# Kernel optimization log

Hardware: AMD Instinct MI355X
Metric: run time of the kernel (lower is better)

Reference implementation:

```python
import jax, jax.numpy as jnp
import numpy as np

S, H, K, B, T = 128, 512, 16, 2048, 67  # state, hidden, bm, batch(paths), len(ts)


def _lin(key, i, o):
    kw, kb = jax.random.split(key)
    w = jax.random.normal(kw, (i, o), jnp.float32) / np.sqrt(i).astype(np.float32)
    b = jax.random.normal(kb, (o,), jnp.float32) * 0.01
    return w, b


def setup_inputs() -> dict:
    key = jax.random.key(0)
    ks = jax.random.split(key, 10)
    enc_w1, enc_b1 = _lin(ks[0], 3, H)
    enc_w2, enc_b2 = _lin(ks[1], H, S)
    f_w1, f_b1 = _lin(ks[2], S + 1, H)
    f_w2, f_b2 = _lin(ks[3], H, H)
    f_w3, f_b3 = _lin(ks[4], H, S)
    g_w1, g_b1 = _lin(ks[5], S + 1, H)
    g_w2, g_b2 = _lin(ks[6], H, S * K)
    ts = jnp.linspace(0.0, 1.0, T, dtype=jnp.float32)
    x = jax.random.normal(ks[7], (B, 3), jnp.float32)
    # standard-normal Brownian increments; scaled by sqrt(dt) inside reference
    dW = jax.random.normal(ks[8], (T - 4, B, K), jnp.float32)
    return dict(ts=ts, x=x,
                enc_w1=enc_w1, enc_b1=enc_b1, enc_w2=enc_w2, enc_b2=enc_b2,
                f_w1=f_w1, f_b1=f_b1, f_w2=f_w2, f_b2=f_b2, f_w3=f_w3, f_b3=f_b3,
                g_w1=g_w1, g_b1=g_b1, g_w2=g_w2, g_b2=g_b2, dW=dW)


def reference(ts, x, enc_w1, enc_b1, enc_w2, enc_b2,
              f_w1, f_b1, f_w2, f_b2, f_w3, f_b3,
              g_w1, g_b1, g_w2, g_b2, dW):
    Bn = x.shape[0]
    Sn = enc_w2.shape[1]
    Kn = dW.shape[-1]

    # encoder: y0 = MLP(x)  -> [B, S]
    y0 = jax.nn.relu(x @ enc_w1 + enc_b1) @ enc_w2 + enc_b2

    ts_sol = ts[3:]                      # solve grid, length T-3
    dts = ts_sol[1:] - ts_sol[:-1]       # [T-4]
    dWs = dW * jnp.sqrt(dts)[:, None, None]  # Brownian increments ~ N(0, dt)

    def with_time(t, y):  # concat scalar time onto state -> [B, S+1]
        tcol = jnp.broadcast_to(jnp.reshape(t, (1, 1)), (Bn, 1)).astype(y.dtype)
        return jnp.concatenate([tcol, y], axis=-1)

    def drift(t, y):  # f(t,y): [B,S]
        h = jax.nn.relu(with_time(t, y) @ f_w1 + f_b1)
        h = jax.nn.relu(h @ f_w2 + f_b2)
        return h @ f_w3 + f_b3

    def g_prod(t, y, dw):  # g(t,y) @ dW : [B,S]
        h = jax.nn.relu(with_time(t, y) @ g_w1 + g_b1)
        g = (h @ g_w2 + g_b2).reshape(Bn, Sn, Kn)
        return jnp.einsum('bsk,bk->bs', g, dw)

    def step(y, inp):  # euler_heun (Stratonovich): Euler drift + Heun diffusion
        t, dt, dw = inp
        gp = g_prod(t, y, dw)
        gp_prime = g_prod(t, y + gp, dw)
        y1 = y + drift(t, y) * dt + 0.5 * (gp + gp_prime)
        return y1, y1

    _, ys = jax.lax.scan(step, y0, (ts_sol[:-1], dts, dWs))
    sol = jnp.concatenate([y0[None], ys], axis=0)  # [T-3, B, S]
    return sol.reshape(-1)
```

## Files before the change

kernel.cpp:

```cpp
#include <hip/hip_runtime.h>
#include <hip/hip_bf16.h>
#include <math.h>

#define B_  2048
#define S_  128
#define H_  512
#define K_  16
#define NSTEP 63

typedef __bf16 bf16x8 __attribute__((ext_vector_type(8)));
typedef float  f32x4  __attribute__((ext_vector_type(4)));
typedef unsigned short u16x8 __attribute__((ext_vector_type(8)));

static __device__ __forceinline__ void f2b2(float v, unsigned short& hi, unsigned short& lo)
{
    __hip_bfloat16 h = __float2bfloat16(v);
    float r = v - __bfloat162float(h);
    __hip_bfloat16 l = __float2bfloat16(r);
    hi = __builtin_bit_cast(unsigned short, h);
    lo = __builtin_bit_cast(unsigned short, l);
}

static __device__ __forceinline__ void gl16(const unsigned short* g, unsigned short* l)
{
    __builtin_amdgcn_global_load_lds(
        (const __attribute__((address_space(1))) unsigned int*)g,
        (__attribute__((address_space(3))) unsigned int*)l, 16, 0, 0);
}

template<int BM,int BN,int BK,int WM,int WN>
__device__ __forceinline__ void gemm_core(
    unsigned short* lds,
    const unsigned short* __restrict__ Ahi, const unsigned short* __restrict__ Alo, int lda,
    const unsigned short* __restrict__ Whi, const unsigned short* __restrict__ Wlo, int K,
    int rowBase, int colBase, f32x4 (&acc)[WM/16][WN/16])
{
    constexpr int MI = WM/16, NJ = WN/16, NWC = BN/WN;
    constexpr int NT = (BM/WM)*(BN/WN)*64;
    constexpr int ACH = BM*BK/8, BCH = BN*BK/8;
    unsigned short* Ah = lds;
    unsigned short* Al = lds + (size_t)ACH*8;
    unsigned short* Bh = lds + (size_t)2*ACH*8;
    unsigned short* Bl = lds + (size_t)2*ACH*8 + (size_t)BCH*8;

    const int tid = threadIdx.x, lane = tid & 63;
    const int wid = tid >> 6;
    const int wr = wid / NWC, wc = wid % NWC;
    const int r16 = lane & 15, kg = lane >> 4;
    const int ubase = tid & ~63;

    for (int k0 = 0; k0 < K; k0 += BK) {
#pragma unroll
        for (int c0 = 0; c0 < ACH; c0 += NT) {
            int c = c0 + tid;
            int row = c % BM, g = c / BM;
            size_t off = (size_t)(rowBase + row) * lda + k0 + g*8;
            gl16(Ahi + off, Ah + (size_t)(c0 + ubase)*8);
            gl16(Alo + off, Al + (size_t)(c0 + ubase)*8);
        }
#pragma unroll
        for (int c0 = 0; c0 < BCH; c0 += NT) {
            int c = c0 + tid;
            int row = c % BN, g = c / BN;
            size_t off = (size_t)(colBase + row) * K + k0 + g*8;
            gl16(Whi + off, Bh + (size_t)(c0 + ubase)*8);
            gl16(Wlo + off, Bl + (size_t)(c0 + ubase)*8);
        }
        __syncthreads();
#pragma unroll
        for (int kk = 0; kk < BK/32; ++kk) {
            bf16x8 ah[MI], al[MI], bh[NJ], bl[NJ];
#pragma unroll
            for (int i = 0; i < MI; ++i) {
                int idx = (kk*4 + kg)*BM + wr*WM + i*16 + r16;
                ah[i] = __builtin_bit_cast(bf16x8, *(const u16x8*)(Ah + (size_t)idx*8));
                al[i] = __builtin_bit_cast(bf16x8, *(const u16x8*)(Al + (size_t)idx*8));
            }
#pragma unroll
            for (int j = 0; j < NJ; ++j) {
                int idx = (kk*4 + kg)*BN + wc*WN + j*16 + r16;
                bh[j] = __builtin_bit_cast(bf16x8, *(const u16x8*)(Bh + (size_t)idx*8));
                bl[j] = __builtin_bit_cast(bf16x8, *(const u16x8*)(Bl + (size_t)idx*8));
            }
#pragma unroll
            for (int i = 0; i < MI; ++i)
#pragma unroll
                for (int j = 0; j < NJ; ++j) {
                    acc[i][j] = __builtin_amdgcn_mfma_f32_16x16x32_bf16(ah[i], bh[j], acc[i][j], 0, 0, 0);
                    acc[i][j] = __builtin_amdgcn_mfma_f32_16x16x32_bf16(ah[i], bl[j], acc[i][j], 0, 0, 0);
                    acc[i][j] = __builtin_amdgcn_mfma_f32_16x16x32_bf16(al[i], bh[j], acc[i][j], 0, 0, 0);
                }
        }
        __syncthreads();
    }
}


__global__ __launch_bounds__(256) void k1_phase(
    const unsigned short* __restrict__ ycH, const unsigned short* __restrict__ ycL,
    const unsigned short* __restrict__ w1tH, const unsigned short* __restrict__ w1tL,
    const float* __restrict__ g_w1, const float* __restrict__ f_w1,
    const float* __restrict__ g_b1, const float* __restrict__ f_b1,
    const float* __restrict__ ts, int step,
    unsigned short* __restrict__ HAh, unsigned short* __restrict__ HAl)
{
    constexpr int BM=64, BN=128, WM=32, WN=64, MI=2, NJ=4, NWC=BN/WN;
    __shared__ __align__(16) unsigned short lds[(BM+BN)*64*2];
    f32x4 acc[MI][NJ] = {};
    const int rowBase = blockIdx.x*BM, colBase = blockIdx.y*BN;
    gemm_core<BM,BN,64,WM,WN>(lds, ycH, ycL, S_, w1tH, w1tL, S_, rowBase, colBase, acc);

    const int tid=threadIdx.x, l=tid&63, wid=tid>>6;
    const int wr=wid/NWC, wc=wid%NWC, r16=l&15, rg=l>>4;
    const float t = ts[3+step];
#pragma unroll
    for (int j=0;j<NJ;++j){
        int colj = colBase + wc*WN + j*16 + r16;
        float be = (colj < 512) ? (g_b1[colj] + t*g_w1[colj])
                                : (f_b1[colj-512] + t*f_w1[colj-512]);
#pragma unroll
        for (int i=0;i<MI;++i)
#pragma unroll
            for (int reg=0;reg<4;++reg){
                int row = rowBase + wr*WM + i*16 + rg*4 + reg;
                float v = fmaxf(acc[i][j][reg] + be, 0.f);
                unsigned short h,lo; f2b2(v,h,lo);
                size_t o = (size_t)row*1024 + colj;
                HAh[o]=h; HAl[o]=lo;
            }
    }
}

__global__ __launch_bounds__(256) void k2_phase(
    const unsigned short* __restrict__ HAh, const unsigned short* __restrict__ HAl,
    const unsigned short* __restrict__ gw2H, const unsigned short* __restrict__ gw2L,
    const unsigned short* __restrict__ fw2H, const unsigned short* __restrict__ fw2L,
    const float* __restrict__ g_b2, const float* __restrict__ f_b2,
    const float* __restrict__ y,
    const float* __restrict__ dWs,
    const float* __restrict__ ts, int step,
    float* __restrict__ gp,
    unsigned short* __restrict__ ytH, unsigned short* __restrict__ ytL,
    unsigned short* __restrict__ HBh, unsigned short* __restrict__ HBl)
{
    constexpr int BM=64, BN=128, WM=32, WN=64, MI=2, NJ=4, NWC=BN/WN;
    __shared__ __align__(16) unsigned short lds[(BM+BN)*64*2];
    f32x4 acc[MI][NJ] = {};
    const int rowBase = blockIdx.x*BM;
    const int by = blockIdx.y;
    const int tid=threadIdx.x, l=tid&63, wid=tid>>6;
    const int wr=wid/NWC, wc=wid%NWC, r16=l&15, rg=l>>4;

    if (by < 16) {
        const int colBase = by*BN;
        gemm_core<BM,BN,64,WM,WN>(lds, HAh, HAl, 1024, gw2H, gw2L, H_, rowBase, colBase, acc);
        const float dt = ts[4+step]-ts[3+step], sq = sqrtf(dt);
#pragma unroll
        for (int i=0;i<MI;++i)
#pragma unroll
            for (int reg=0;reg<4;++reg){
                int row = rowBase + wr*WM + i*16 + rg*4 + reg;
                float dwv = dWs[row*K_ + r16] * sq;
#pragma unroll
                for (int j=0;j<NJ;++j){
                    int colj = colBase + wc*WN + j*16;
                    float m = (acc[i][j][reg] + g_b2[colj + r16]) * dwv;
                    m += __shfl_xor(m,1); m += __shfl_xor(m,2);
                    m += __shfl_xor(m,4); m += __shfl_xor(m,8);
                    if (r16 == 0){
                        int idx = row*S_ + (colj>>4);
                        gp[idx] = m;
                        unsigned short h,lo; f2b2(y[idx] + m, h, lo);
                        ytH[idx]=h; ytL[idx]=lo;
                    }
                }
            }
    } else {
        const int colBase = (by-16)*BN;
        gemm_core<BM,BN,64,WM,WN>(lds, HAh + 512, HAl + 512, 1024, fw2H, fw2L, H_, rowBase, colBase, acc);
#pragma unroll
        for (int j=0;j<NJ;++j){
            int colj = colBase + wc*WN + j*16 + r16;
            float be = f_b2[colj];
#pragma unroll
            for (int i=0;i<MI;++i)
#pragma unroll
                for (int reg=0;reg<4;++reg){
                    int row = rowBase + wr*WM + i*16 + rg*4 + reg;
                    float v = fmaxf(acc[i][j][reg] + be, 0.f);
                    unsigned short h,lo; f2b2(v,h,lo);
                    size_t o = (size_t)row*512 + colj;
                    HBh[o]=h; HBl[o]=lo;
                }
        }
    }
}

__global__ __launch_bounds__(256) void k3_phase(
    const unsigned short* __restrict__ ytH, const unsigned short* __restrict__ ytL,
    const unsigned short* __restrict__ w1tH, const unsigned short* __restrict__ w1tL,
    const float* __restrict__ g_b1, const float* __restrict__ g_w1,
    const unsigned short* __restrict__ HBh, const unsigned short* __restrict__ HBl,
    const unsigned short* __restrict__ fw3H, const unsigned short* __restrict__ fw3L,
    const float* __restrict__ f_b3,
    const float* __restrict__ ts, int step,
    unsigned short* __restrict__ HA2h, unsigned short* __restrict__ HA2l,
    float* __restrict__ drift)
{
    constexpr int BM=64, BN=64, WM=32, WN=32, MI=2, NJ=2, NWC=BN/WN;
    __shared__ __align__(16) unsigned short lds[(BM+BN)*64*2];
    f32x4 acc[MI][NJ] = {};
    const int rowBase = blockIdx.x*BM;
    const int by = blockIdx.y;
    const int tid=threadIdx.x, l=tid&63, wid=tid>>6;
    const int wr=wid/NWC, wc=wid%NWC, r16=l&15, rg=l>>4;

    if (by < 8) {
        const int colBase = by*BN;
        gemm_core<BM,BN,64,WM,WN>(lds, ytH, ytL, S_, w1tH, w1tL, S_, rowBase, colBase, acc);
        const float t = ts[3+step];
#pragma unroll
        for (int j=0;j<NJ;++j){
            int colj = colBase + wc*WN + j*16 + r16;
            float be = g_b1[colj] + t*g_w1[colj];
#pragma unroll
            for (int i=0;i<MI;++i)
#pragma unroll
                for (int reg=0;reg<4;++reg){
                    int row = rowBase + wr*WM + i*16 + rg*4 + reg;
                    float v = fmaxf(acc[i][j][reg] + be, 0.f);
                    unsigned short h,lo; f2b2(v,h,lo);
                    size_t o = (size_t)row*512 + colj;
                    HA2h[o]=h; HA2l[o]=lo;
                }
        }
    } else {
        const int colBase = (by-8)*BN;
        gemm_core<BM,BN,64,WM,WN>(lds, HBh, HBl, H_, fw3H, fw3L, H_, rowBase, colBase, acc);
#pragma unroll
        for (int j=0;j<NJ;++j){
            int colj = colBase + wc*WN + j*16 + r16;
            float be = f_b3[colj];
#pragma unroll
            for (int i=0;i<MI;++i)
#pragma unroll
                for (int reg=0;reg<4;++reg){
                    int row = rowBase + wr*WM + i*16 + rg*4 + reg;
                    drift[row*S_ + colj] = acc[i][j][reg] + be;
                }
        }
    }
}

__global__ __launch_bounds__(256) void k4_phase(
    const unsigned short* __restrict__ HA2h, const unsigned short* __restrict__ HA2l,
    const unsigned short* __restrict__ gw2H, const unsigned short* __restrict__ gw2L,
    const float* __restrict__ g_b2,
    const float* __restrict__ y,
    const float* __restrict__ gp,
    const float* __restrict__ drift,
    const float* __restrict__ dWs,
    const float* __restrict__ ts, int step,
    float* __restrict__ y1,
    unsigned short* __restrict__ ycH, unsigned short* __restrict__ ycL)
{
    constexpr int BM=64, BN=128, WM=32, WN=64, MI=2, NJ=4, NWC=BN/WN;
    __shared__ __align__(16) unsigned short lds[(BM+BN)*64*2];
    f32x4 acc[MI][NJ] = {};
    const int rowBase = blockIdx.x*BM;
    const int colBase = blockIdx.y*BN;
    gemm_core<BM,BN,64,WM,WN>(lds, HA2h, HA2l, H_, gw2H, gw2L, H_, rowBase, colBase, acc);

    const int tid=threadIdx.x, l=tid&63, wid=tid>>6;
    const int wr=wid/NWC, wc=wid%NWC, r16=l&15, rg=l>>4;
    const float dt = ts[4+step]-ts[3+step], sq = sqrtf(dt);
#pragma unroll
    for (int i=0;i<MI;++i)
#pragma unroll
        for (int reg=0;reg<4;++reg){
            int row = rowBase + wr*WM + i*16 + rg*4 + reg;
            float dwv = dWs[row*K_ + r16] * sq;
#pragma unroll
            for (int j=0;j<NJ;++j){
                int colj = colBase + wc*WN + j*16;
                float m = (acc[i][j][reg] + g_b2[colj + r16]) * dwv;
                m += __shfl_xor(m,1); m += __shfl_xor(m,2);
                m += __shfl_xor(m,4); m += __shfl_xor(m,8);
                if (r16 == 0){
                    int idx = row*S_ + (colj>>4);
                    float v1 = y[idx] + drift[idx]*dt + 0.5f*(gp[idx] + m);
                    y1[idx] = v1;
                    unsigned short h,lo; f2b2(v1,h,lo);
                    ycH[idx]=h; ycL[idx]=lo;
                }
            }
        }
}

__global__ __launch_bounds__(256) void tcast_k(
    const float* __restrict__ in, int rowOff, int Kd, int N,
    unsigned short* __restrict__ outH, unsigned short* __restrict__ outL)
{
    __shared__ float tl[32][33];
    const int kb = blockIdx.x*32, nb = blockIdx.y*32;
    const int tx = threadIdx.x, ty = threadIdx.y;
    for (int r = ty; r < 32; r += 8)
        tl[r][tx] = in[(size_t)(rowOff + kb + r)*N + nb + tx];
    __syncthreads();
    for (int r = ty; r < 32; r += 8){
        unsigned short h,lo; f2b2(tl[tx][r],h,lo);
        size_t o = (size_t)(nb + r)*Kd + kb + tx;
        outH[o]=h; outL[o]=lo;
    }
}

__global__ __launch_bounds__(128) void encoder_k(
    const float* __restrict__ x,
    const float* __restrict__ w1, const float* __restrict__ b1,
    const float* __restrict__ w2, const float* __restrict__ b2,
    float* __restrict__ y0,
    unsigned short* __restrict__ ycH, unsigned short* __restrict__ ycL)
{
    int b = blockIdx.x;
    __shared__ float h[H_];
    int tid = threadIdx.x;
    float x0 = x[b*3+0], x1 = x[b*3+1], x2 = x[b*3+2];
    for (int i = tid; i < H_; i += 128)
        h[i] = fmaxf(x0*w1[i] + x1*w1[H_+i] + x2*w1[2*H_+i] + b1[i], 0.f);
    __syncthreads();
    float acc = b2[tid];
    for (int k = 0; k < H_; ++k) acc += h[k]*w2[k*S_+tid];
    size_t o = (size_t)b*S_ + tid;
    y0[o] = acc;
    unsigned short hh,ll; f2b2(acc,hh,ll);
    ycH[o]=hh; ycL[o]=ll;
}

extern "C" void kernel_launch(void* const* d_in, const int* in_sizes, int n_in,
                              void* d_out, int out_size, void* d_ws, size_t ws_size,
                              hipStream_t stream)
{
    const float* ts     = (const float*)d_in[0];
    const float* x      = (const float*)d_in[1];
    const float* enc_w1 = (const float*)d_in[2];
    const float* enc_b1 = (const float*)d_in[3];
    const float* enc_w2 = (const float*)d_in[4];
    const float* enc_b2 = (const float*)d_in[5];
    const float* f_w1   = (const float*)d_in[6];
    const float* f_b1   = (const float*)d_in[7];
    const float* f_w2   = (const float*)d_in[8];
    const float* f_b2   = (const float*)d_in[9];
    const float* f_w3   = (const float*)d_in[10];
    const float* f_b3   = (const float*)d_in[11];
    const float* g_w1   = (const float*)d_in[12];
    const float* g_b1   = (const float*)d_in[13];
    const float* g_w2   = (const float*)d_in[14];
    const float* g_b2   = (const float*)d_in[15];
    const float* dW     = (const float*)d_in[16];

    float* out = (float*)d_out;
    unsigned short* w = (unsigned short*)d_ws;

    unsigned short* w1tH  = w;
    unsigned short* w1tL  = w1tH  + 1024*128;
    unsigned short* gw2H  = w1tL  + 1024*128;
    unsigned short* gw2L  = gw2H  + 2048*512;
    unsigned short* fw2H  = gw2L  + 2048*512;
    unsigned short* fw2L  = fw2H  + 512*512;
    unsigned short* fw3H  = fw2L  + 512*512;
    unsigned short* fw3L  = fw3H  + 128*512;
    unsigned short* HAh   = fw3L  + 128*512;
    unsigned short* HAl   = HAh   + 2048*1024;
    unsigned short* HBh   = HAl   + 2048*1024;
    unsigned short* HBl   = HBh   + 2048*512;
    unsigned short* ytH   = HBl   + 2048*512;
    unsigned short* ytL   = ytH   + 2048*128;
    unsigned short* ycH   = ytL   + 2048*128;
    unsigned short* ycL   = ycH   + 2048*128;
    float* gp    = (float*)(ycL + 2048*128);
    float* drift = gp + 2048*128;
    unsigned short* HA2h = HAh;
    unsigned short* HA2l = HAl;

    dim3 tb(32,8);
    tcast_k<<<dim3(4,16),  tb, 0, stream>>>(g_w1, 1, 128, 512,  w1tH,          w1tL);
    tcast_k<<<dim3(4,16),  tb, 0, stream>>>(f_w1, 1, 128, 512,  w1tH+512*128,  w1tL+512*128);
    tcast_k<<<dim3(16,16), tb, 0, stream>>>(f_w2, 0, 512, 512,  fw2H,          fw2L);
    tcast_k<<<dim3(16,4),  tb, 0, stream>>>(f_w3, 0, 512, 128,  fw3H,          fw3L);
    tcast_k<<<dim3(16,64), tb, 0, stream>>>(g_w2, 0, 512, 2048, gw2H,          gw2L);

    encoder_k<<<B_, 128, 0, stream>>>(x, enc_w1, enc_b1, enc_w2, enc_b2, out, ycH, ycL);

    for (int step = 0; step < NSTEP; ++step) {
        const float* y   = out + (size_t)step * B_ * S_;
        float*       y1  = out + (size_t)(step+1) * B_ * S_;
        const float* dWs = dW  + (size_t)step * B_ * K_;

        k1_phase<<<dim3(32,8),  256, 0, stream>>>(ycH, ycL, w1tH, w1tL, g_w1, f_w1,
                                                  g_b1, f_b1, ts, step, HAh, HAl);
        k2_phase<<<dim3(32,20), 256, 0, stream>>>(HAh, HAl, gw2H, gw2L, fw2H, fw2L,
                                                  g_b2, f_b2, y, dWs, ts, step,
                                                  gp, ytH, ytL, HBh, HBl);
        k3_phase<<<dim3(32,10), 256, 0, stream>>>(ytH, ytL, w1tH, w1tL, g_b1, g_w1,
                                                  HBh, HBl, fw3H, fw3L, f_b3, ts, step,
                                                  HA2h, HA2l, drift);
        k4_phase<<<dim3(32,16), 256, 0, stream>>>(HA2h, HA2l, gw2H, gw2L, g_b2,
                                                  y, gp, drift, dWs, ts, step,
                                                  y1, ycH, ycL);
    }
}
```

Before: 7.322 ms.

## Double-buffer LDS tiles in GEMM core, enlarge tiles, swizzle block order

Rewrites the shared split-bf16 GEMM core to double-buffer LDS tiles, issuing the next K-tile's global-to-LDS loads while MFMAs run on the current one, with one barrier per tile. The k2 and k4 GEMMs move to 128x128 tiles, k3 uses 64x128 tiles, and all launches become 1D grids remapped so consecutive blocks spread across column strips. The aim is to hide global-load latency and improve weight reuse in L2. In exchange it doubles LDS use and sets launch_bounds to one block per CU, and the larger tiles give k2 and k4 fewer blocks than before.

Measured after the change: 10.34 ms. 1.41x slower.

```diff
diff --git a/kernel.cpp b/kernel.cpp
--- a/kernel.cpp
+++ b/kernel.cpp
@@ -28,75 +28,110 @@
         (__attribute__((address_space(3))) unsigned int*)l, 16, 0, 0);
 }
 
-template<int BM,int BN,int BK,int WM,int WN>
-__device__ __forceinline__ void gemm_core(
+
+template<int BM>
+static __device__ __forceinline__ void stage_tile(
+    const unsigned short* __restrict__ Ahi, const unsigned short* __restrict__ Alo, int lda,
+    const unsigned short* __restrict__ Whi, const unsigned short* __restrict__ Wlo, int K,
+    int rowBase, int colBase, int k0, unsigned short* buf, int tid)
+{
+    constexpr int PLA = BM*64, PLB = 128*64;
+    unsigned short* Ah = buf;
+    unsigned short* Al = buf + PLA;
+    unsigned short* Bh = buf + 2*PLA;
+    unsigned short* Bl = buf + 2*PLA + PLB;
+    const int ub = tid & ~63;
+#pragma unroll
+    for (int c0 = 0; c0 < BM*8; c0 += 256) {
+        int c = c0 + tid;
+        int row = c % BM, g = c / BM;
+        size_t off = (size_t)(rowBase + row) * lda + k0 + g*8;
+        gl16(Ahi + off, Ah + (size_t)(c0 + ub)*8);
+        gl16(Alo + off, Al + (size_t)(c0 + ub)*8);
+    }
+#pragma unroll
+    for (int c0 = 0; c0 < 1024; c0 += 256) {
+        int c = c0 + tid;
+        int row = c & 127, g = c >> 7;
+        size_t off = (size_t)(colBase + row) * K + k0 + g*8;
+        gl16(Whi + off, Bh + (size_t)(c0 + ub)*8);
+        gl16(Wlo + off, Bl + (size_t)(c0 + ub)*8);
+    }
+}
+
+template<int BM>
+static __device__ __forceinline__ void read_frags(
+    const unsigned short* buf, int kk, int wr, int wc, int r16, int kg,
+    bf16x8 (&a_h)[BM/32], bf16x8 (&a_l)[BM/32], bf16x8 (&b_h)[4], bf16x8 (&b_l)[4])
+{
+    constexpr int MI = BM/32;
+    constexpr int PLA = BM*64, PLB = 128*64;
+    const unsigned short* Ah = buf;
+    const unsigned short* Al = buf + PLA;
+    const unsigned short* Bh = buf + 2*PLA;
+    const unsigned short* Bl = buf + 2*PLA + PLB;
+#pragma unroll
+    for (int i = 0; i < MI; ++i) {
+        int ch = (kk*4 + kg)*BM + wr*(BM/2) + i*16 + r16;
+        a_h[i] = __builtin_bit_cast(bf16x8, *(const u16x8*)(Ah + (size_t)ch*8));
+        a_l[i] = __builtin_bit_cast(bf16x8, *(const u16x8*)(Al + (size_t)ch*8));
+    }
+#pragma unroll
+    for (int j = 0; j < 4; ++j) {
+        int ch = (kk*4 + kg)*128 + wc*64 + j*16 + r16;
+        b_h[j] = __builtin_bit_cast(bf16x8, *(const u16x8*)(Bh + (size_t)ch*8));
+        b_l[j] = __builtin_bit_cast(bf16x8, *(const u16x8*)(Bl + (size_t)ch*8));
+    }
+}
+
+template<int MI>
+static __device__ __forceinline__ void do_mfma(
+    const bf16x8 (&a_h)[MI], const bf16x8 (&a_l)[MI],
+    const bf16x8 (&b_h)[4], const bf16x8 (&b_l)[4], f32x4 (&acc)[MI][4])
+{
+#pragma unroll
+    for (int i = 0; i < MI; ++i)
+#pragma unroll
+        for (int j = 0; j < 4; ++j) {
+            acc[i][j] = __builtin_amdgcn_mfma_f32_16x16x32_bf16(a_h[i], b_h[j], acc[i][j], 0, 0, 0);
+            acc[i][j] = __builtin_amdgcn_mfma_f32_16x16x32_bf16(a_h[i], b_l[j], acc[i][j], 0, 0, 0);
+            acc[i][j] = __builtin_amdgcn_mfma_f32_16x16x32_bf16(a_l[i], b_h[j], acc[i][j], 0, 0, 0);
+        }
+}
+
+template<int BM>
+static __device__ __forceinline__ void gemm_core(
     unsigned short* lds,
     const unsigned short* __restrict__ Ahi, const unsigned short* __restrict__ Alo, int lda,
     const unsigned short* __restrict__ Whi, const unsigned short* __restrict__ Wlo, int K,
-    int rowBase, int colBase, f32x4 (&acc)[WM/16][WN/16])
-{
-    constexpr int MI = WM/16, NJ = WN/16, NWC = BN/WN;
-    constexpr int NT = (BM/WM)*(BN/WN)*64;
-    constexpr int ACH = BM*BK/8, BCH = BN*BK/8;
-    unsigned short* Ah = lds;
-    unsigned short* Al = lds + (size_t)ACH*8;
-    unsigned short* Bh = lds + (size_t)2*ACH*8;
-    unsigned short* Bl = lds + (size_t)2*ACH*8 + (size_t)BCH*8;
-
+    int rowBase, int colBase, f32x4 (&acc)[BM/32][4])
+{
+    constexpr int MI = BM/32;
+    constexpr int BUFSZ = 2*BM*64 + 2*128*64;
     const int tid = threadIdx.x, lane = tid & 63;
-    const int wid = tid >> 6;
-    const int wr = wid / NWC, wc = wid % NWC;
+    const int wid = tid >> 6, wr = wid >> 1, wc = wid & 1;
     const int r16 = lane & 15, kg = lane >> 4;
-    const int ubase = tid & ~63;
-
-    for (int k0 = 0; k0 < K; k0 += BK) {
-#pragma unroll
-        for (int c0 = 0; c0 < ACH; c0 += NT) {
-            int c = c0 + tid;
-            int row = c % BM, g = c / BM;
-            size_t off = (size_t)(rowBase + row) * lda + k0 + g*8;
-            gl16(Ahi + off, Ah + (size_t)(c0 + ubase)*8);
-            gl16(Alo + off, Al + (size_t)(c0 + ubase)*8);
-        }
-#pragma unroll
-        for (int c0 = 0; c0 < BCH; c0 += NT) {
-            int c = c0 + tid;
-            int row = c % BN, g = c / BN;
-            size_t off = (size_t)(colBase + row) * K + k0 + g*8;
-            gl16(Whi + off, Bh + (size_t)(c0 + ubase)*8);
-            gl16(Wlo + off, Bl + (size_t)(c0 + ubase)*8);
-        }
+
+    const int nt = K >> 6;
+    stage_tile<BM>(Ahi, Alo, lda, Whi, Wlo, K, rowBase, colBase, 0, lds, tid);
+    __syncthreads();
+
+    for (int t = 0; t < nt; ++t) {
+        unsigned short* cur = lds + (size_t)(t & 1) * BUFSZ;
+        bf16x8 a_h[MI], a_l[MI], b_h[4], b_l[4];
+        read_frags<BM>(cur, 0, wr, wc, r16, kg, a_h, a_l, b_h, b_l);
+        if (t + 1 < nt)
+            stage_tile<BM>(Ahi, Alo, lda, Whi, Wlo, K, rowBase, colBase, (t+1) << 6,
+                           lds + (size_t)((t+1) & 1) * BUFSZ, tid);
+        do_mfma<MI>(a_h, a_l, b_h, b_l, acc);
+        read_frags<BM>(cur, 1, wr, wc, r16, kg, a_h, a_l, b_h, b_l);
+        do_mfma<MI>(a_h, a_l, b_h, b_l, acc);
         __syncthreads();
-#pragma unroll
-        for (int kk = 0; kk < BK/32; ++kk) {
-            bf16x8 ah[MI], al[MI], bh[NJ], bl[NJ];
-#pragma unroll
-            for (int i = 0; i < MI; ++i) {
-                int idx = (kk*4 + kg)*BM + wr*WM + i*16 + r16;
-                ah[i] = __builtin_bit_cast(bf16x8, *(const u16x8*)(Ah + (size_t)idx*8));
-                al[i] = __builtin_bit_cast(bf16x8, *(const u16x8*)(Al + (size_t)idx*8));
-            }
-#pragma unroll
-            for (int j = 0; j < NJ; ++j) {
-                int idx = (kk*4 + kg)*BN + wc*WN + j*16 + r16;
-                bh[j] = __builtin_bit_cast(bf16x8, *(const u16x8*)(Bh + (size_t)idx*8));
-                bl[j] = __builtin_bit_cast(bf16x8, *(const u16x8*)(Bl + (size_t)idx*8));
-            }
-#pragma unroll
-            for (int i = 0; i < MI; ++i)
-#pragma unroll
-                for (int j = 0; j < NJ; ++j) {
-                    acc[i][j] = __builtin_amdgcn_mfma_f32_16x16x32_bf16(ah[i], bh[j], acc[i][j], 0, 0, 0);
-                    acc[i][j] = __builtin_amdgcn_mfma_f32_16x16x32_bf16(ah[i], bl[j], acc[i][j], 0, 0, 0);
-                    acc[i][j] = __builtin_amdgcn_mfma_f32_16x16x32_bf16(al[i], bh[j], acc[i][j], 0, 0, 0);
-                }
-        }
-        __syncthreads();
-    }
-}
-
-
-__global__ __launch_bounds__(256) void k1_phase(
+    }
+}
+
+
+__global__ __launch_bounds__(256,1) void k1_phase(
     const unsigned short* __restrict__ ycH, const unsigned short* __restrict__ ycL,
     const unsigned short* __restrict__ w1tH, const unsigned short* __restrict__ w1tL,
     const float* __restrict__ g_w1, const float* __restrict__ f_w1,
@@ -104,25 +139,29 @@
     const float* __restrict__ ts, int step,
     unsigned short* __restrict__ HAh, unsigned short* __restrict__ HAl)
 {
-    constexpr int BM=64, BN=128, WM=32, WN=64, MI=2, NJ=4, NWC=BN/WN;
-    __shared__ __align__(16) unsigned short lds[(BM+BN)*64*2];
-    f32x4 acc[MI][NJ] = {};
-    const int rowBase = blockIdx.x*BM, colBase = blockIdx.y*BN;
-    gemm_core<BM,BN,64,WM,WN>(lds, ycH, ycL, S_, w1tH, w1tL, S_, rowBase, colBase, acc);
+    constexpr int BM=64, MI=2;
+    __shared__ __align__(16) unsigned short lds[2*(2*BM*64 + 2*128*64)];
+    const int bid = blockIdx.x;
+    const int lid = (bid & 7)*32 + (bid >> 3);
+    const int strip = lid >> 5, rowb = lid & 31;
+    const int rowBase = rowb*BM, colBase = strip*128;
+
+    f32x4 acc[MI][4] = {};
+    gemm_core<BM>(lds, ycH, ycL, S_, w1tH, w1tL, S_, rowBase, colBase, acc);
 
     const int tid=threadIdx.x, l=tid&63, wid=tid>>6;
-    const int wr=wid/NWC, wc=wid%NWC, r16=l&15, rg=l>>4;
+    const int wr=wid>>1, wc=wid&1, r16=l&15, rg=l>>4;
     const float t = ts[3+step];
 #pragma unroll
-    for (int j=0;j<NJ;++j){
-        int colj = colBase + wc*WN + j*16 + r16;
+    for (int j=0;j<4;++j){
+        int colj = colBase + wc*64 + j*16 + r16;
         float be = (colj < 512) ? (g_b1[colj] + t*g_w1[colj])
                                 : (f_b1[colj-512] + t*f_w1[colj-512]);
 #pragma unroll
         for (int i=0;i<MI;++i)
 #pragma unroll
             for (int reg=0;reg<4;++reg){
-                int row = rowBase + wr*WM + i*16 + rg*4 + reg;
+                int row = rowBase + wr*(BM/2) + i*16 + rg*4 + reg;
                 float v = fmaxf(acc[i][j][reg] + be, 0.f);
                 unsigned short h,lo; f2b2(v,h,lo);
                 size_t o = (size_t)row*1024 + colj;
@@ -131,7 +170,7 @@
     }
 }
 
-__global__ __launch_bounds__(256) void k2_phase(
+__global__ __launch_bounds__(256,1) void k2_phase(
     const unsigned short* __restrict__ HAh, const unsigned short* __restrict__ HAl,
     const unsigned short* __restrict__ gw2H, const unsigned short* __restrict__ gw2L,
     const unsigned short* __restrict__ fw2H, const unsigned short* __restrict__ fw2L,
@@ -143,27 +182,30 @@
     unsigned short* __restrict__ ytH, unsigned short* __restrict__ ytL,
     unsigned short* __restrict__ HBh, unsigned short* __restrict__ HBl)
 {
-    constexpr int BM=64, BN=128, WM=32, WN=64, MI=2, NJ=4, NWC=BN/WN;
-    __shared__ __align__(16) unsigned short lds[(BM+BN)*64*2];
-    f32x4 acc[MI][NJ] = {};
-    const int rowBase = blockIdx.x*BM;
-    const int by = blockIdx.y;
+    constexpr int BM=128, MI=4;
+    __shared__ __align__(16) unsigned short lds[2*(2*BM*64 + 2*128*64)];
+    const int bid = blockIdx.x;
+    const int lid = (bid & 7)*40 + (bid >> 3);
+    const int strip = lid >> 4, rowb = lid & 15;
+    const int rowBase = rowb*BM;
+
     const int tid=threadIdx.x, l=tid&63, wid=tid>>6;
-    const int wr=wid/NWC, wc=wid%NWC, r16=l&15, rg=l>>4;
-
-    if (by < 16) {
-        const int colBase = by*BN;
-        gemm_core<BM,BN,64,WM,WN>(lds, HAh, HAl, 1024, gw2H, gw2L, H_, rowBase, colBase, acc);
+    const int wr=wid>>1, wc=wid&1, r16=l&15, rg=l>>4;
+
+    f32x4 acc[MI][4] = {};
+    if (strip < 16) {
+        const int colBase = strip*128;
+        gemm_core<BM>(lds, HAh, HAl, 1024, gw2H, gw2L, H_, rowBase, colBase, acc);
         const float dt = ts[4+step]-ts[3+step], sq = sqrtf(dt);
 #pragma unroll
         for (int i=0;i<MI;++i)
 #pragma unroll
             for (int reg=0;reg<4;++reg){
-                int row = rowBase + wr*WM + i*16 + rg*4 + reg;
+                int row = rowBase + wr*(BM/2) + i*16 + rg*4 + reg;
                 float dwv = dWs[row*K_ + r16] * sq;
 #pragma unroll
-                for (int j=0;j<NJ;++j){
-                    int colj = colBase + wc*WN + j*16;
+                for (int j=0;j<4;++j){
+                    int colj = colBase + wc*64 + j*16;
                     float m = (acc[i][j][reg] + g_b2[colj + r16]) * dwv;
                     m += __shfl_xor(m,1); m += __shfl_xor(m,2);
                     m += __shfl_xor(m,4); m += __shfl_xor(m,8);
@@ -176,17 +218,17 @@
                 }
             }
     } else {
-        const int colBase = (by-16)*BN;
-        gemm_core<BM,BN,64,WM,WN>(lds, HAh + 512, HAl + 512, 1024, fw2H, fw2L, H_, rowBase, colBase, acc);
-#pragma unroll
-        for (int j=0;j<NJ;++j){
-            int colj = colBase + wc*WN + j*16 + r16;
+        const int colBase = (strip-16)*128;
+        gemm_core<BM>(lds, HAh + 512, HAl + 512, 1024, fw2H, fw2L, H_, rowBase, colBase, acc);
+#pragma unroll
+        for (int j=0;j<4;++j){
+            int colj = colBase + wc*64 + j*16 + r16;
             float be = f_b2[colj];
 #pragma unroll
             for (int i=0;i<MI;++i)
 #pragma unroll
                 for (int reg=0;reg<4;++reg){
-                    int row = rowBase + wr*WM + i*16 + rg*4 + reg;
+                    int row = rowBase + wr*(BM/2) + i*16 + rg*4 + reg;
                     float v = fmaxf(acc[i][j][reg] + be, 0.f);
                     unsigned short h,lo; f2b2(v,h,lo);
                     size_t o = (size_t)row*512 + colj;
@@ -196,7 +238,7 @@
     }
 }
 
-__global__ __launch_bounds__(256) void k3_phase(
+__global__ __launch_bounds__(256,1) void k3_phase(
     const unsigned short* __restrict__ ytH, const unsigned short* __restrict__ ytL,
     const unsigned short* __restrict__ w1tH, const unsigned short* __restrict__ w1tL,
     const float* __restrict__ g_b1, const float* __restrict__ g_w1,
@@ -207,27 +249,30 @@
     unsigned short* __restrict__ HA2h, unsigned short* __restrict__ HA2l,
     float* __restrict__ drift)
 {
-    constexpr int BM=64, BN=64, WM=32, WN=32, MI=2, NJ=2, NWC=BN/WN;
-    __shared__ __align__(16) unsigned short lds[(BM+BN)*64*2];
-    f32x4 acc[MI][NJ] = {};
-    const int rowBase = blockIdx.x*BM;
-    const int by = blockIdx.y;
+    constexpr int BM=64, MI=2;
+    __shared__ __align__(16) unsigned short lds[2*(2*BM*64 + 2*128*64)];
+    const int bid = blockIdx.x;
+    const int lid = (bid & 7)*20 + (bid >> 3);
+    const int strip = lid >> 5, rowb = lid & 31;
+    const int rowBase = rowb*BM;
+
     const int tid=threadIdx.x, l=tid&63, wid=tid>>6;
-    const int wr=wid/NWC, wc=wid%NWC, r16=l&15, rg=l>>4;
-
-    if (by < 8) {
-        const int colBase = by*BN;
-        gemm_core<BM,BN,64,WM,WN>(lds, ytH, ytL, S_, w1tH, w1tL, S_, rowBase, colBase, acc);
+    const int wr=wid>>1, wc=wid&1, r16=l&15, rg=l>>4;
+
+    f32x4 acc[MI][4] = {};
+    if (strip < 4) {
+        const int colBase = strip*128;
+        gemm_core<BM>(lds, ytH, ytL, S_, w1tH, w1tL, S_, rowBase, colBase, acc);
         const float t = ts[3+step];
 #pragma unroll
-        for (int j=0;j<NJ;++j){
-            int colj = colBase + wc*WN + j*16 + r16;
+        for (int j=0;j<4;++j){
+            int colj = colBase + wc*64 + j*16 + r16;
             float be = g_b1[colj] + t*g_w1[colj];
 #pragma unroll
             for (int i=0;i<MI;++i)
 #pragma unroll
                 for (int reg=0;reg<4;++reg){
-                    int row = rowBase + wr*WM + i*16 + rg*4 + reg;
+                    int row = rowBase + wr*(BM/2) + i*16 + rg*4 + reg;
                     float v = fmaxf(acc[i][j][reg] + be, 0.f);
                     unsigned short h,lo; f2b2(v,h,lo);
                     size_t o = (size_t)row*512 + colj;
@@ -235,24 +280,23 @@
                 }
         }
     } else {
-        const int colBase = (by-8)*BN;
-        gemm_core<BM,BN,64,WM,WN>(lds, HBh, HBl, H_, fw3H, fw3L, H_, rowBase, colBase, acc);
-#pragma unroll
-        for (int j=0;j<NJ;++j){
-            int colj = colBase + wc*WN + j*16 + r16;
+        gemm_core<BM>(lds, HBh, HBl, H_, fw3H, fw3L, H_, rowBase, 0, acc);
+#pragma unroll
+        for (int j=0;j<4;++j){
+            int colj = wc*64 + j*16 + r16;
             float be = f_b3[colj];
 #pragma unroll
             for (int i=0;i<MI;++i)
 #pragma unroll
                 for (int reg=0;reg<4;++reg){
-                    int row = rowBase + wr*WM + i*16 + rg*4 + reg;
+                    int row = rowBase + wr*(BM/2) + i*16 + rg*4 + reg;
                     drift[row*S_ + colj] = acc[i][j][reg] + be;
                 }
         }
     }
 }
 
-__global__ __launch_bounds__(256) void k4_phase(
+__global__ __launch_bounds__(256,1) void k4_phase(
     const unsigned short* __restrict__ HA2h, const unsigned short* __restrict__ HA2l,
     const unsigned short* __restrict__ gw2H, const unsigned short* __restrict__ gw2L,
     const float* __restrict__ g_b2,
@@ -264,25 +308,28 @@
     float* __restrict__ y1,
     unsigned short* __restrict__ ycH, unsigned short* __restrict__ ycL)
 {
-    constexpr int BM=64, BN=128, WM=32, WN=64, MI=2, NJ=4, NWC=BN/WN;
-    __shared__ __align__(16) unsigned short lds[(BM+BN)*64*2];
-    f32x4 acc[MI][NJ] = {};
-    const int rowBase = blockIdx.x*BM;
-    const int colBase = blockIdx.y*BN;
-    gemm_core<BM,BN,64,WM,WN>(lds, HA2h, HA2l, H_, gw2H, gw2L, H_, rowBase, colBase, acc);
+    constexpr int BM=128, MI=4;
+    __shared__ __align__(16) unsigned short lds[2*(2*BM*64 + 2*128*64)];
+    const int bid = blockIdx.x;
+    const int lid = (bid & 7)*32 + (bid >> 3);
+    const int strip = lid >> 4, rowb = lid & 15;
+    const int rowBase = rowb*BM, colBase = strip*128;
+
+    f32x4 acc[MI][4] = {};
+    gemm_core<BM>(lds, HA2h, HA2l, H_, gw2H, gw2L, H_, rowBase, colBase, acc);
 
     const int tid=threadIdx.x, l=tid&63, wid=tid>>6;
-    const int wr=wid/NWC, wc=wid%NWC, r16=l&15, rg=l>>4;
+    const int wr=wid>>1, wc=wid&1, r16=l&15, rg=l>>4;
     const float dt = ts[4+step]-ts[3+step], sq = sqrtf(dt);
 #pragma unroll
     for (int i=0;i<MI;++i)
 #pragma unroll
         for (int reg=0;reg<4;++reg){
-            int row = rowBase + wr*WM + i*16 + rg*4 + reg;
+            int row = rowBase + wr*(BM/2) + i*16 + rg*4 + reg;
             float dwv = dWs[row*K_ + r16] * sq;
 #pragma unroll
-            for (int j=0;j<NJ;++j){
-                int colj = colBase + wc*WN + j*16;
+            for (int j=0;j<4;++j){
+                int colj = colBase + wc*64 + j*16;
                 float m = (acc[i][j][reg] + g_b2[colj + r16]) * dwv;
                 m += __shfl_xor(m,1); m += __shfl_xor(m,2);
                 m += __shfl_xor(m,4); m += __shfl_xor(m,8);
@@ -396,16 +443,16 @@
         float*       y1  = out + (size_t)(step+1) * B_ * S_;
         const float* dWs = dW  + (size_t)step * B_ * K_;
 
-        k1_phase<<<dim3(32,8),  256, 0, stream>>>(ycH, ycL, w1tH, w1tL, g_w1, f_w1,
-                                                  g_b1, f_b1, ts, step, HAh, HAl);
-        k2_phase<<<dim3(32,20), 256, 0, stream>>>(HAh, HAl, gw2H, gw2L, fw2H, fw2L,
-                                                  g_b2, f_b2, y, dWs, ts, step,
-                                                  gp, ytH, ytL, HBh, HBl);
-        k3_phase<<<dim3(32,10), 256, 0, stream>>>(ytH, ytL, w1tH, w1tL, g_b1, g_w1,
-                                                  HBh, HBl, fw3H, fw3L, f_b3, ts, step,
-                                                  HA2h, HA2l, drift);
-        k4_phase<<<dim3(32,16), 256, 0, stream>>>(HA2h, HA2l, gw2H, gw2L, g_b2,
-                                                  y, gp, drift, dWs, ts, step,
-                                                  y1, ycH, ycL);
-    }
-}
+        k1_phase<<<256, 256, 0, stream>>>(ycH, ycL, w1tH, w1tL, g_w1, f_w1,
+                                          g_b1, f_b1, ts, step, HAh, HAl);
+        k2_phase<<<320, 256, 0, stream>>>(HAh, HAl, gw2H, gw2L, fw2H, fw2L,
+                                          g_b2, f_b2, y, dWs, ts, step,
+                                          gp, ytH, ytL, HBh, HBl);
+        k3_phase<<<160, 256, 0, stream>>>(ytH, ytL, w1tH, w1tL, g_b1, g_w1,
+                                          HBh, HBl, fw3H, fw3L, f_b3, ts, step,
+                                          HA2h, HA2l, drift);
+        k4_phase<<<256, 256, 0, stream>>>(HA2h, HA2l, gw2H, gw2L, g_b2,
+                                          y, gp, drift, dWs, ts, step,
+                                          y1, ycH, ycL);
+    }
+}
```
